# Optimization experiments

Hardware: AMD Instinct MI355X
Metric: run time of the kernel (lower is better)

Reference implementation:

```python
import jax, jax.numpy as jnp
import numpy as np

B, S, H = 2, 2048, 1024
N_HEADS = 16
HEAD_DIM = H // N_HEADS


def setup_inputs() -> dict:
    key = jax.random.key(0)
    ks = jax.random.split(key, 7)
    scale = 0.02
    return {
        "q": jax.random.normal(ks[0], (B, S, H), dtype=jnp.float32),
        "k": jax.random.normal(ks[1], (B, S, H), dtype=jnp.float32),
        "v": jax.random.normal(ks[2], (B, S, H), dtype=jnp.float32),
        "Wq": jax.random.normal(ks[3], (H, H), dtype=jnp.float32) * scale,
        "Wk": jax.random.normal(ks[4], (H, H), dtype=jnp.float32) * scale,
        "Wv": jax.random.normal(ks[5], (H, H), dtype=jnp.float32) * scale,
        "Wo": jax.random.normal(ks[6], (H, H), dtype=jnp.float32) * scale,
    }


def reference(q, k, v, Wq, Wk, Wv, Wo):
    b, i, _ = q.shape
    _, j, _ = k.shape
    # torch.nn.Linear(bias=False): y = x @ W.T
    qp = q @ Wq.T
    kp = k @ Wk.T
    vp = v @ Wv.T
    # NOTE: original uses .view(b, n_heads, i, head_dim) with NO transpose,
    # i.e. a raw reshape of the (b, i, hidden) layout. Replicate exactly.
    qh = qp.reshape(b, N_HEADS, i, HEAD_DIM)
    kh = kp.reshape(b, N_HEADS, j, HEAD_DIM)
    vh = vp.reshape(b, N_HEADS, j, HEAD_DIM)
    attn_score = jnp.einsum("bnid,bnjd->bnij", qh, kh) / (HEAD_DIM ** 0.5)
    attn_weight = jax.nn.softmax(attn_score, axis=3)
    x = jnp.einsum("bnij,bnjd->bnid", attn_weight, vh)  # [b, n, i, d]
    # rearrange 'b n i d -> b i (n d)'
    x = jnp.transpose(x, (0, 2, 1, 3)).reshape(b, i, H)
    out = x @ Wo.T
    return (out, attn_weight)
```

## Files before the change

kernel.cpp:

```cpp
#include <hip/hip_runtime.h>
#include <hip/hip_bf16.h>

#define DEVI __device__ __forceinline__

constexpr int kS  = 2048;
constexpr int kH  = 1024;
constexpr int kD  = 64;
constexpr int kBS = 4096;
constexpr int kHeadEls = kS * kD;

typedef __attribute__((ext_vector_type(4))) float f32x4;
typedef __attribute__((ext_vector_type(8))) __bf16 bf16x8;
typedef __attribute__((ext_vector_type(8))) unsigned short u16x8;
typedef __attribute__((ext_vector_type(2))) unsigned int u32x2;

DEVI unsigned short f2bf(float f) {
  unsigned int u = __builtin_bit_cast(unsigned int, f);
  u = u + 0x7FFFu + ((u >> 16) & 1u);
  return (unsigned short)(u >> 16);
}
DEVI float fast_exp2(float x) { float r; asm("v_exp_f32 %0, %1" : "=v"(r) : "v"(x)); return r; }
DEVI unsigned int cvt_pk(float lo, float hi) {
  unsigned int r; asm("v_cvt_pk_bf16_f32 %0, %1, %2" : "=v"(r) : "v"(lo), "v"(hi)); return r;
}
DEVI bf16x8 cvt8(const f32x4 a, const f32x4 b) {
  union { unsigned int u[4]; bf16x8 v; } r;
  r.u[0] = cvt_pk(a[0], a[1]); r.u[1] = cvt_pk(a[2], a[3]);
  r.u[2] = cvt_pk(b[0], b[1]); r.u[3] = cvt_pk(b[2], b[3]);
  return r.v;
}
DEVI float bf2f(unsigned int lo16) {
  return __builtin_bit_cast(float, lo16 << 16);
}

#define GLDS16(g, l) __builtin_amdgcn_global_load_lds( \
    (const __attribute__((address_space(1))) void*)(g), \
    (__attribute__((address_space(3))) void*)(l), 16, 0, 0)

__global__ __launch_bounds__(256) void cvt_all(
    const float* __restrict__ q, const float* __restrict__ k, const float* __restrict__ v,
    const float* __restrict__ Wq, const float* __restrict__ Wk, const float* __restrict__ Wv,
    unsigned short* __restrict__ stash)
{
  const int z = blockIdx.y, x = blockIdx.x;
  const float* s;
  unsigned short* d;
  size_t i;
  if (x < 2048) {
    s = z == 0 ? q : z == 1 ? k : v;
    d = stash + (size_t)z * 4194304;
    i = ((size_t)x * 256 + threadIdx.x) * 8;
  } else {
    s = z == 0 ? Wq : z == 1 ? Wk : Wv;
    d = stash + (size_t)12582912 + (size_t)z * 1048576;
    i = ((size_t)(x - 2048) * 256 + threadIdx.x) * 8;
  }
  f32x4 a = *(const f32x4*)(s + i);
  f32x4 b = *(const f32x4*)(s + i + 4);
  union { unsigned int u[4]; u16x8 v; } r;
  r.u[0] = cvt_pk(a[0], a[1]); r.u[1] = cvt_pk(a[2], a[3]);
  r.u[2] = cvt_pk(b[0], b[1]); r.u[3] = cvt_pk(b[2], b[3]);
  *(u16x8*)(d + i) = r.v;
}

__global__ __launch_bounds__(256, 3) void gemm_p(
    const unsigned short* __restrict__ Aq, const unsigned short* __restrict__ Ak,
    const unsigned short* __restrict__ Av,
    const unsigned short* __restrict__ Bq, const unsigned short* __restrict__ Bk,
    const unsigned short* __restrict__ Bv,
    unsigned short* __restrict__ Cq, unsigned short* __restrict__ Ck,
    unsigned short* __restrict__ Cv)
{
  constexpr int K = kH;
  __shared__ __align__(16) unsigned char As[2][8192];
  __shared__ __align__(16) unsigned char Bs[2][8192];

  const int z = blockIdx.z;
  const unsigned short* Ap = z == 0 ? Aq : z == 1 ? Ak : Av;
  const unsigned short* Bp = z == 0 ? Bq : z == 1 ? Bk : Bv;
  unsigned short*       Cp = z == 0 ? Cq : z == 1 ? Ck : Cv;

  const int tid  = threadIdx.x;
  const int lane = tid & 63, wv = tid >> 6;
  const int l15  = lane & 15, lg = lane >> 4;
  const int m0 = blockIdx.y * 128, n0 = blockIdx.x * 128;
  const int wM = (wv & 1) * 64, wN = (wv >> 1) * 64;

  const char* aSrc[2];
  const char* bSrc[2];
#pragma unroll
  for (int c = 0; c < 2; ++c) {
    const int row = c * 64 + (tid >> 2);
    const int cb  = ((tid & 3) * 16) ^ (((row >> 1) & 3) << 4);
    aSrc[c] = (const char*)Ap + ((size_t)(m0 + row) * K) * 2 + cb;
    bSrc[c] = (const char*)Bp + ((size_t)(n0 + row) * K) * 2 + cb;
  }

  int aoff[4], boff[4];
#pragma unroll
  for (int t = 0; t < 4; ++t) {
    const int rA = wM + t * 16 + l15;
    aoff[t] = rA * 64 + ((lg * 16) ^ (((rA >> 1) & 3) << 4));
    const int rB = wN + t * 16 + l15;
    boff[t] = rB * 64 + ((lg * 16) ^ (((rB >> 1) & 3) << 4));
  }

  f32x4 acc[4][4];
#pragma unroll
  for (int i = 0; i < 4; ++i)
#pragma unroll
    for (int j = 0; j < 4; ++j) acc[i][j] = {0.f, 0.f, 0.f, 0.f};

  auto STG = [&](int kk, int bb) {
#pragma unroll
    for (int c = 0; c < 2; ++c) {
      GLDS16(aSrc[c] + (size_t)kk * 2, &As[bb][c * 4096 + wv * 1024]);
      GLDS16(bSrc[c] + (size_t)kk * 2, &Bs[bb][c * 4096 + wv * 1024]);
    }
  };

  STG(0, 0);
  __syncthreads();
  int cur = 0;
  for (int t = 0; t < K / 32; ++t) {
    if (t < K / 32 - 1) STG((t + 1) * 32, cur ^ 1);
    bf16x8 af[4], bfr[4];
#pragma unroll
    for (int x = 0; x < 4; ++x) {
      af[x]  = *(const bf16x8*)&As[cur][aoff[x]];
      bfr[x] = *(const bf16x8*)&Bs[cur][boff[x]];
    }
#pragma unroll
    for (int mt = 0; mt < 4; ++mt)
#pragma unroll
      for (int nt = 0; nt < 4; ++nt)
        acc[mt][nt] = __builtin_amdgcn_mfma_f32_16x16x32_bf16(af[mt], bfr[nt], acc[mt][nt], 0, 0, 0);
    __syncthreads();
    cur ^= 1;
  }

  const bool vmode = (z == 2);
#pragma unroll
  for (int mt = 0; mt < 4; ++mt)
#pragma unroll
    for (int nt = 0; nt < 4; ++nt)
#pragma unroll
      for (int r = 0; r < 4; ++r) {
        const int row = m0 + wM + mt * 16 + lg * 4 + r;
        const int col = n0 + wN + nt * 16 + l15;
        const unsigned short hv = f2bf(acc[mt][nt][r]);
        if (!vmode) {
          Cp[(size_t)row * kH + col] = hv;
        } else {
          const int bn = row >> 7;
          const int j  = ((row & 127) << 4) | (col >> 6);
          const int d  = col & 63;
          Cp[(size_t)bn * kHeadEls + (size_t)d * kS + j] = hv;
        }
      }
}

__global__ __launch_bounds__(256, 3) void gemm_f(
    const unsigned short* __restrict__ Ap, const float* __restrict__ Bp,
    float* __restrict__ Cp)
{
  constexpr int K = kH;
  __shared__ __align__(16) unsigned char As[2][8192];
  __shared__ __align__(16) unsigned char Bs[2][8192];

  const int tid  = threadIdx.x;
  const int lane = tid & 63, wv = tid >> 6;
  const int l15  = lane & 15, lg = lane >> 4;
  const int m0 = blockIdx.y * 128, n0 = blockIdx.x * 64;
  const int wM = (wv & 1) * 64, wN = (wv >> 1) * 32;

  const char* aSrc[2];
#pragma unroll
  for (int c = 0; c < 2; ++c) {
    const int row = c * 64 + (tid >> 2);
    const int cb  = ((tid & 3) * 16) ^ (((row >> 1) & 3) << 4);
    aSrc[c] = (const char*)Ap + ((size_t)(m0 + row) * K) * 2 + cb;
  }
  const char* bSrc[2];
#pragma unroll
  for (int c = 0; c < 2; ++c) {
    const int row = c * 32 + (tid >> 3);
    const int cb  = ((tid & 7) * 16) ^ ((row & 7) << 4);
    bSrc[c] = (const char*)Bp + ((size_t)(n0 + row) * K) * 4 + cb;
  }

  int aoff[4], boff[2];
#pragma unroll
  for (int t = 0; t < 4; ++t) {
    const int rA = wM + t * 16 + l15;
    aoff[t] = rA * 64 + ((lg * 16) ^ (((rA >> 1) & 3) << 4));
  }
#pragma unroll
  for (int t = 0; t < 2; ++t) {
    const int rB = wN + t * 16 + l15;
    boff[t] = rB * 128 + ((lg * 32) ^ ((rB & 7) << 4));
  }

  f32x4 acc[4][2];
#pragma unroll
  for (int i = 0; i < 4; ++i)
#pragma unroll
    for (int j = 0; j < 2; ++j) acc[i][j] = {0.f, 0.f, 0.f, 0.f};

  auto STG = [&](int kk, int bb) {
#pragma unroll
    for (int c = 0; c < 2; ++c) {
      GLDS16(aSrc[c] + (size_t)kk * 2, &As[bb][c * 4096 + wv * 1024]);
      GLDS16(bSrc[c] + (size_t)kk * 4, &Bs[bb][c * 4096 + wv * 1024]);
    }
  };

  STG(0, 0);
  __syncthreads();
  int cur = 0;
  for (int t = 0; t < K / 32; ++t) {
    if (t < K / 32 - 1) STG((t + 1) * 32, cur ^ 1);
    bf16x8 af[4], bfr[2];
#pragma unroll
    for (int x = 0; x < 4; ++x)
      af[x] = *(const bf16x8*)&As[cur][aoff[x]];
#pragma unroll
    for (int x = 0; x < 2; ++x) {
      f32x4 q0 = *(const f32x4*)&Bs[cur][boff[x]];
      f32x4 q1 = *(const f32x4*)&Bs[cur][boff[x] ^ 16];
      bfr[x] = cvt8(q0, q1);
    }
#pragma unroll
    for (int mt = 0; mt < 4; ++mt)
#pragma unroll
      for (int nt = 0; nt < 2; ++nt)
        acc[mt][nt] = __builtin_amdgcn_mfma_f32_16x16x32_bf16(af[mt], bfr[nt], acc[mt][nt], 0, 0, 0);
    __syncthreads();
    cur ^= 1;
  }

#pragma unroll
  for (int mt = 0; mt < 4; ++mt)
#pragma unroll
    for (int nt = 0; nt < 2; ++nt)
#pragma unroll
      for (int r = 0; r < 4; ++r) {
        const int row = m0 + wM + mt * 16 + lg * 4 + r;
        const int col = n0 + wN + nt * 16 + l15;
        __builtin_nontemporal_store(acc[mt][nt][r], Cp + (size_t)row * kH + col);
      }
}

__global__ __launch_bounds__(256, 2) void attn_rs(
    const unsigned short* __restrict__ QP,
    const unsigned short* __restrict__ KP,
    float* __restrict__ rsout)
{
  __shared__ __align__(16) unsigned short Kb[2][4096];

  const int tid  = threadIdx.x;
  const int lane = tid & 63, wv = tid >> 6;
  const int l15  = lane & 15, lg = lane >> 4;
  const int f = blockIdx.x;
  const int x = f & 7, r = f >> 3;
  const int bn = (r >> 4) * 8 + x;
  const int i0 = (r & 15) * 128;

  const char* Khb = (const char*)(KP + (size_t)bn * kHeadEls);
  const unsigned short* Qh = QP + (size_t)bn * kHeadEls;

  int kbase[2];
#pragma unroll
  for (int p = 0; p < 2; ++p) {
    const int row = p * 32 + (tid >> 3);
    kbase[p] = row * 128 + (((tid & 7) * 16) ^ ((row & 7) << 4));
  }
  auto STAGE = [&](int j0, int bb) {
#pragma unroll
    for (int p = 0; p < 2; ++p)
      GLDS16(Khb + (size_t)j0 * 128 + kbase[p], (char*)Kb[bb] + p * 4096 + tid * 16);
  };

  int koff[4][2];
#pragma unroll
  for (int ct = 0; ct < 4; ++ct) {
    const int rK = ct * 16 + l15;
#pragma unroll
    for (int h = 0; h < 2; ++h)
      koff[ct][h] = rK * 128 + ((h * 64 + lg * 16) ^ ((rK & 7) << 4));
  }

  bf16x8 qf[2][2];
#pragma unroll
  for (int m = 0; m < 2; ++m) {
    const int qr = i0 + wv * 32 + m * 16 + l15;
#pragma unroll
    for (int h = 0; h < 2; ++h)
      qf[m][h] = *(const bf16x8*)(Qh + (size_t)qr * kD + h * 32 + lg * 8);
  }
  const float cexp = 0.18033688011112042f;

  float rs[2] = {0.f, 0.f};
  STAGE(0, 0);
  __syncthreads();
  int cur = 0;
  for (int t = 0; t < 32; ++t) {
    if (t < 31) STAGE((t + 1) * 64, cur ^ 1);
#pragma unroll
    for (int ct = 0; ct < 4; ++ct) {
      const bf16x8 kb0 = *(const bf16x8*)((const char*)Kb[cur] + koff[ct][0]);
      const bf16x8 kb1 = *(const bf16x8*)((const char*)Kb[cur] + koff[ct][1]);
#pragma unroll
      for (int m = 0; m < 2; ++m) {
        f32x4 s = {0.f, 0.f, 0.f, 0.f};
        s = __builtin_amdgcn_mfma_f32_16x16x32_bf16(kb0, qf[m][0], s, 0, 0, 0);
        s = __builtin_amdgcn_mfma_f32_16x16x32_bf16(kb1, qf[m][1], s, 0, 0, 0);
        const float w0 = fast_exp2(s[0] * cexp), w1 = fast_exp2(s[1] * cexp);
        const float w2 = fast_exp2(s[2] * cexp), w3 = fast_exp2(s[3] * cexp);
        rs[m] += (w0 + w1) + (w2 + w3);
      }
    }
    __syncthreads();
    cur ^= 1;
  }
#pragma unroll
  for (int m = 0; m < 2; ++m) {
    rs[m] += __shfl_xor(rs[m], 16, 64);
    rs[m] += __shfl_xor(rs[m], 32, 64);
  }
  if (lg == 0) {
#pragma unroll
    for (int m = 0; m < 2; ++m)
      rsout[(size_t)bn * kS + i0 + wv * 32 + m * 16 + l15] = rs[m];
  }
}

__global__ __launch_bounds__(256, 3) void attn_main(
    const unsigned short* __restrict__ QP,
    const unsigned short* __restrict__ KP,
    const unsigned short* __restrict__ VPT,
    const float* __restrict__ rsb,
    float* __restrict__ AW,
    unsigned short* __restrict__ XB)
{
  __shared__ __align__(16) unsigned short Kb[2][4096];
  __shared__ __align__(16) unsigned short Vb[2][4096];
  __shared__ __align__(16) unsigned short Ws[8192];

  const int tid  = threadIdx.x;
  const int lane = tid & 63, wv = tid >> 6;
  const int l15  = lane & 15, lg = lane >> 4;
  const int f = blockIdx.x;
  const int x = f & 7, r = f >> 3;
  const int bn = (r >> 4) * 8 + x;
  const int i0 = (r & 15) * 128;
  const int b = bn >> 4, n = bn & 15;

  const char* Khb = (const char*)(KP + (size_t)bn * kHeadEls);
  const char* Vhb = (const char*)(VPT + (size_t)bn * kHeadEls);
  const unsigned short* Qh = QP + (size_t)bn * kHeadEls;

  int kbase[2], vbase[2];
#pragma unroll
  for (int p = 0; p < 2; ++p) {
    const int row = p * 32 + (tid >> 3);
    const int sw  = ((tid & 7) * 16) ^ ((row & 7) << 4);
    kbase[p] = row * 128 + sw;
    vbase[p] = row * 4096 + sw;
  }
  auto STAGE_KV = [&](int j0, int bb) {
#pragma unroll
    for (int p = 0; p < 2; ++p) {
      GLDS16(Khb + (size_t)j0 * 128 + kbase[p], (char*)Kb[bb] + p * 4096 + tid * 16);
      GLDS16(Vhb + (size_t)j0 * 2 + vbase[p],   (char*)Vb[bb] + p * 4096 + tid * 16);
    }
  };

  int koff[4][2], voff[2][4], wswr[2][4], wsrd[2][2];
#pragma unroll
  for (int ct = 0; ct < 4; ++ct) {
    const int rK = ct * 16 + l15;
#pragma unroll
    for (int h = 0; h < 2; ++h)
      koff[ct][h] = rK * 128 + ((h * 64 + lg * 16) ^ ((rK & 7) << 4));
  }
#pragma unroll
  for (int jc = 0; jc < 2; ++jc)
#pragma unroll
    for (int dt = 0; dt < 4; ++dt) {
      const int d = dt * 16 + l15;
      voff[jc][dt] = d * 128 + ((jc * 64 + lg * 16) ^ ((d & 7) << 4));
    }
#pragma unroll
  for (int m = 0; m < 2; ++m) {
    const int rw = wv * 32 + m * 16 + l15;
#pragma unroll
    for (int ct = 0; ct < 4; ++ct)
      wswr[m][ct] = rw * 128 + ((ct * 32 + lg * 8) ^ ((rw & 7) << 4));
#pragma unroll
    for (int jc = 0; jc < 2; ++jc)
      wsrd[m][jc] = rw * 128 + ((jc * 64 + lg * 16) ^ ((rw & 7) << 4));
  }

  int awrd[8];
  float* awp[8];
#pragma unroll
  for (int u = 0; u < 8; ++u) {
    const int rw = wv * 32 + u * 4 + lg;
    awrd[u] = rw * 128 + ((l15 * 8) ^ ((rw & 7) << 4));
    awp[u]  = AW + ((size_t)bn * kS + i0 + rw) * kS + l15 * 4;
  }

  bf16x8 qf[2][2];
  float inv[2];
#pragma unroll
  for (int m = 0; m < 2; ++m) {
    const int qr = i0 + wv * 32 + m * 16 + l15;
#pragma unroll
    for (int h = 0; h < 2; ++h)
      qf[m][h] = *(const bf16x8*)(Qh + (size_t)qr * kD + h * 32 + lg * 8);
    inv[m] = 1.0f / rsb[(size_t)bn * kS + qr];
  }
  const float cexp = 0.18033688011112042f;

  f32x4 pv[2][4];
#pragma unroll
  for (int m = 0; m < 2; ++m)
#pragma unroll
    for (int dt = 0; dt < 4; ++dt) pv[m][dt] = {0.f, 0.f, 0.f, 0.f};

  STAGE_KV(0, 0);
  asm volatile("s_waitcnt vmcnt(0) lgkmcnt(0)" ::: "memory");
  __builtin_amdgcn_sched_barrier(0);
  __builtin_amdgcn_s_barrier();

  int cur = 0;
  for (int t = 0; t < 32; ++t) {
    if (t < 31) STAGE_KV((t + 1) * 64, cur ^ 1);
    __builtin_amdgcn_sched_barrier(0);
#pragma unroll
    for (int ct = 0; ct < 4; ++ct) {
      const bf16x8 kb0 = *(const bf16x8*)((const char*)Kb[cur] + koff[ct][0]);
      const bf16x8 kb1 = *(const bf16x8*)((const char*)Kb[cur] + koff[ct][1]);
#pragma unroll
      for (int m = 0; m < 2; ++m) {
        f32x4 s = {0.f, 0.f, 0.f, 0.f};
        s = __builtin_amdgcn_mfma_f32_16x16x32_bf16(kb0, qf[m][0], s, 0, 0, 0);
        s = __builtin_amdgcn_mfma_f32_16x16x32_bf16(kb1, qf[m][1], s, 0, 0, 0);
        f32x4 w;
#pragma unroll
        for (int r2 = 0; r2 < 4; ++r2) w[r2] = fast_exp2(s[r2] * cexp) * inv[m];
        u32x2 pk; pk[0] = cvt_pk(w[0], w[1]); pk[1] = cvt_pk(w[2], w[3]);
        *(u32x2*)((char*)Ws + wswr[m][ct]) = pk;
      }
    }
#pragma unroll
    for (int jc = 0; jc < 2; ++jc) {
      const bf16x8 pa0 = *(const bf16x8*)((const char*)Ws + wsrd[0][jc]);
      const bf16x8 pa1 = *(const bf16x8*)((const char*)Ws + wsrd[1][jc]);
#pragma unroll
      for (int dt = 0; dt < 4; ++dt) {
        const bf16x8 vf = *(const bf16x8*)((const char*)Vb[cur] + voff[jc][dt]);
        pv[0][dt] = __builtin_amdgcn_mfma_f32_16x16x32_bf16(pa0, vf, pv[0][dt], 0, 0, 0);
        pv[1][dt] = __builtin_amdgcn_mfma_f32_16x16x32_bf16(pa1, vf, pv[1][dt], 0, 0, 0);
      }
    }
#pragma unroll
    for (int u = 0; u < 8; ++u) {
      const u32x2 pk = *(const u32x2*)((const char*)Ws + awrd[u]);
      f32x4 w;
      w[0] = bf2f(pk[0] & 0xFFFFu);
      w[1] = bf2f(pk[0] >> 16);
      w[2] = bf2f(pk[1] & 0xFFFFu);
      w[3] = bf2f(pk[1] >> 16);
      __builtin_nontemporal_store(w, (f32x4*)(awp[u] + t * 64));
    }
    if (t < 31) {
      asm volatile("s_waitcnt vmcnt(8) lgkmcnt(0)" ::: "memory");
      __builtin_amdgcn_sched_barrier(0);
      __builtin_amdgcn_s_barrier();
    }
    cur ^= 1;
  }

#pragma unroll
  for (int m = 0; m < 2; ++m)
#pragma unroll
    for (int dt = 0; dt < 4; ++dt)
#pragma unroll
      for (int r2 = 0; r2 < 4; ++r2) {
        const int row = b * kS + i0 + wv * 32 + m * 16 + lg * 4 + r2;
        const int col = n * 64 + dt * 16 + l15;
        XB[(size_t)row * kH + col] = f2bf(pv[m][dt][r2]);
      }
}

extern "C" void kernel_launch(void* const* d_in, const int* in_sizes, int n_in,
                              void* d_out, int out_size, void* d_ws, size_t ws_size,
                              hipStream_t stream) {
  const float* q  = (const float*)d_in[0];
  const float* k  = (const float*)d_in[1];
  const float* v  = (const float*)d_in[2];
  const float* Wq = (const float*)d_in[3];
  const float* Wk = (const float*)d_in[4];
  const float* Wv = (const float*)d_in[5];
  const float* Wo = (const float*)d_in[6];

  float* out = (float*)d_out;
  float* aw  = out + (size_t)kBS * kH;
  float* rsb = out;

  unsigned short* QP  = (unsigned short*)d_ws;
  unsigned short* KP  = QP  + (size_t)kBS * kH;
  unsigned short* VPT = KP  + (size_t)kBS * kH;
  unsigned short* XB  = VPT + (size_t)kBS * kH;

  unsigned short* stash = (unsigned short*)aw;
  unsigned short* QB  = stash;
  unsigned short* KB  = stash + (size_t)4194304;
  unsigned short* VB  = stash + (size_t)8388608;
  unsigned short* Wqb = stash + (size_t)12582912;
  unsigned short* Wkb = stash + (size_t)13631488;
  unsigned short* Wvb = stash + (size_t)14680064;

  cvt_all<<<dim3(2560, 3), 256, 0, stream>>>(q, k, v, Wq, Wk, Wv, stash);
  gemm_p<<<dim3(8, 32, 3), 256, 0, stream>>>(QB, KB, VB, Wqb, Wkb, Wvb, QP, KP, VPT);
  attn_rs<<<dim3(512), 256, 0, stream>>>(QP, KP, rsb);
  attn_main<<<dim3(512), 256, 0, stream>>>(QP, KP, VPT, rsb, aw, XB);
  gemm_f<<<dim3(16, 32), 256, 0, stream>>>(XB, Wo, out);
}
```

Measured before the change: 247.5 us.

## Fuse row-sum pass into attention kernel and triple-buffer GEMM staging

Merges the separate softmax row-sum kernel into the main attention kernel. Each block now first sweeps K in 128-row tiles through a triple-buffered LDS region to compute its own row sums, then reuses the same shared memory for the K/V/weights pass, which removes one launch and the global round trip of the row sums. Both projection GEMMs switch from double to triple buffering, issuing loads two tiles ahead and waiting with a partial vmcnt instead of a full __syncthreads. The cost is higher LDS use (48KB per block), which may reduce occupancy, and a longer serial section per attention block.

```diff
diff --git a/kernel.cpp b/kernel.cpp
--- a/kernel.cpp
+++ b/kernel.cpp
@@ -36,6 +36,11 @@
 #define GLDS16(g, l) __builtin_amdgcn_global_load_lds( \
     (const __attribute__((address_space(1))) void*)(g), \
     (__attribute__((address_space(3))) void*)(l), 16, 0, 0)
+
+#define WAIT_VM(n) do { \
+    asm volatile("s_waitcnt vmcnt(" #n ") lgkmcnt(0)" ::: "memory"); \
+    __builtin_amdgcn_sched_barrier(0); \
+    __builtin_amdgcn_s_barrier(); } while (0)
 
 __global__ __launch_bounds__(256) void cvt_all(
     const float* __restrict__ q, const float* __restrict__ k, const float* __restrict__ v,
@@ -72,8 +77,8 @@
     unsigned short* __restrict__ Cv)
 {
   constexpr int K = kH;
-  __shared__ __align__(16) unsigned char As[2][8192];
-  __shared__ __align__(16) unsigned char Bs[2][8192];
+  __shared__ __align__(16) unsigned char As[3][8192];
+  __shared__ __align__(16) unsigned char Bs[3][8192];
 
   const int z = blockIdx.z;
   const unsigned short* Ap = z == 0 ? Aq : z == 1 ? Ak : Av;
@@ -119,11 +124,11 @@
     }
   };
 
-  STG(0, 0);
-  __syncthreads();
-  int cur = 0;
-  for (int t = 0; t < K / 32; ++t) {
-    if (t < K / 32 - 1) STG((t + 1) * 32, cur ^ 1);
+  STG(0, 0); STG(32, 1);
+  WAIT_VM(4);
+  int cur = 0, nx2 = 2;
+  for (int t = 0; t < 32; ++t) {
+    if (t < 30) STG((t + 2) * 32, nx2);
     bf16x8 af[4], bfr[4];
 #pragma unroll
     for (int x = 0; x < 4; ++x) {
@@ -135,8 +140,12 @@
 #pragma unroll
       for (int nt = 0; nt < 4; ++nt)
         acc[mt][nt] = __builtin_amdgcn_mfma_f32_16x16x32_bf16(af[mt], bfr[nt], acc[mt][nt], 0, 0, 0);
-    __syncthreads();
-    cur ^= 1;
+    if (t < 31) {
+      if (t < 30) WAIT_VM(4);
+      else        WAIT_VM(0);
+    }
+    cur = cur == 2 ? 0 : cur + 1;
+    nx2 = nx2 == 2 ? 0 : nx2 + 1;
   }
 
   const bool vmode = (z == 2);
@@ -165,8 +174,8 @@
     float* __restrict__ Cp)
 {
   constexpr int K = kH;
-  __shared__ __align__(16) unsigned char As[2][8192];
-  __shared__ __align__(16) unsigned char Bs[2][8192];
+  __shared__ __align__(16) unsigned char As[3][8192];
+  __shared__ __align__(16) unsigned char Bs[3][8192];
 
   const int tid  = threadIdx.x;
   const int lane = tid & 63, wv = tid >> 6;
@@ -215,11 +224,11 @@
     }
   };
 
-  STG(0, 0);
-  __syncthreads();
-  int cur = 0;
-  for (int t = 0; t < K / 32; ++t) {
-    if (t < K / 32 - 1) STG((t + 1) * 32, cur ^ 1);
+  STG(0, 0); STG(32, 1);
+  WAIT_VM(4);
+  int cur = 0, nx2 = 2;
+  for (int t = 0; t < 32; ++t) {
+    if (t < 30) STG((t + 2) * 32, nx2);
     bf16x8 af[4], bfr[2];
 #pragma unroll
     for (int x = 0; x < 4; ++x)
@@ -235,8 +244,12 @@
 #pragma unroll
       for (int nt = 0; nt < 2; ++nt)
         acc[mt][nt] = __builtin_amdgcn_mfma_f32_16x16x32_bf16(af[mt], bfr[nt], acc[mt][nt], 0, 0, 0);
-    __syncthreads();
-    cur ^= 1;
+    if (t < 31) {
+      if (t < 30) WAIT_VM(4);
+      else        WAIT_VM(0);
+    }
+    cur = cur == 2 ? 0 : cur + 1;
+    nx2 = nx2 == 2 ? 0 : nx2 + 1;
   }
 
 #pragma unroll
@@ -251,101 +264,14 @@
       }
 }
 
-__global__ __launch_bounds__(256, 2) void attn_rs(
-    const unsigned short* __restrict__ QP,
-    const unsigned short* __restrict__ KP,
-    float* __restrict__ rsout)
-{
-  __shared__ __align__(16) unsigned short Kb[2][4096];
-
-  const int tid  = threadIdx.x;
-  const int lane = tid & 63, wv = tid >> 6;
-  const int l15  = lane & 15, lg = lane >> 4;
-  const int f = blockIdx.x;
-  const int x = f & 7, r = f >> 3;
-  const int bn = (r >> 4) * 8 + x;
-  const int i0 = (r & 15) * 128;
-
-  const char* Khb = (const char*)(KP + (size_t)bn * kHeadEls);
-  const unsigned short* Qh = QP + (size_t)bn * kHeadEls;
-
-  int kbase[2];
-#pragma unroll
-  for (int p = 0; p < 2; ++p) {
-    const int row = p * 32 + (tid >> 3);
-    kbase[p] = row * 128 + (((tid & 7) * 16) ^ ((row & 7) << 4));
-  }
-  auto STAGE = [&](int j0, int bb) {
-#pragma unroll
-    for (int p = 0; p < 2; ++p)
-      GLDS16(Khb + (size_t)j0 * 128 + kbase[p], (char*)Kb[bb] + p * 4096 + tid * 16);
-  };
-
-  int koff[4][2];
-#pragma unroll
-  for (int ct = 0; ct < 4; ++ct) {
-    const int rK = ct * 16 + l15;
-#pragma unroll
-    for (int h = 0; h < 2; ++h)
-      koff[ct][h] = rK * 128 + ((h * 64 + lg * 16) ^ ((rK & 7) << 4));
-  }
-
-  bf16x8 qf[2][2];
-#pragma unroll
-  for (int m = 0; m < 2; ++m) {
-    const int qr = i0 + wv * 32 + m * 16 + l15;
-#pragma unroll
-    for (int h = 0; h < 2; ++h)
-      qf[m][h] = *(const bf16x8*)(Qh + (size_t)qr * kD + h * 32 + lg * 8);
-  }
-  const float cexp = 0.18033688011112042f;
-
-  float rs[2] = {0.f, 0.f};
-  STAGE(0, 0);
-  __syncthreads();
-  int cur = 0;
-  for (int t = 0; t < 32; ++t) {
-    if (t < 31) STAGE((t + 1) * 64, cur ^ 1);
-#pragma unroll
-    for (int ct = 0; ct < 4; ++ct) {
-      const bf16x8 kb0 = *(const bf16x8*)((const char*)Kb[cur] + koff[ct][0]);
-      const bf16x8 kb1 = *(const bf16x8*)((const char*)Kb[cur] + koff[ct][1]);
-#pragma unroll
-      for (int m = 0; m < 2; ++m) {
-        f32x4 s = {0.f, 0.f, 0.f, 0.f};
-        s = __builtin_amdgcn_mfma_f32_16x16x32_bf16(kb0, qf[m][0], s, 0, 0, 0);
-        s = __builtin_amdgcn_mfma_f32_16x16x32_bf16(kb1, qf[m][1], s, 0, 0, 0);
-        const float w0 = fast_exp2(s[0] * cexp), w1 = fast_exp2(s[1] * cexp);
-        const float w2 = fast_exp2(s[2] * cexp), w3 = fast_exp2(s[3] * cexp);
-        rs[m] += (w0 + w1) + (w2 + w3);
-      }
-    }
-    __syncthreads();
-    cur ^= 1;
-  }
-#pragma unroll
-  for (int m = 0; m < 2; ++m) {
-    rs[m] += __shfl_xor(rs[m], 16, 64);
-    rs[m] += __shfl_xor(rs[m], 32, 64);
-  }
-  if (lg == 0) {
-#pragma unroll
-    for (int m = 0; m < 2; ++m)
-      rsout[(size_t)bn * kS + i0 + wv * 32 + m * 16 + l15] = rs[m];
-  }
-}
-
-__global__ __launch_bounds__(256, 3) void attn_main(
+__global__ __launch_bounds__(256, 3) void attn_fused(
     const unsigned short* __restrict__ QP,
     const unsigned short* __restrict__ KP,
     const unsigned short* __restrict__ VPT,
-    const float* __restrict__ rsb,
     float* __restrict__ AW,
     unsigned short* __restrict__ XB)
 {
-  __shared__ __align__(16) unsigned short Kb[2][4096];
-  __shared__ __align__(16) unsigned short Vb[2][4096];
-  __shared__ __align__(16) unsigned short Ws[8192];
+  __shared__ __align__(16) unsigned char SM[49152];
 
   const int tid  = threadIdx.x;
   const int lane = tid & 63, wv = tid >> 6;
@@ -360,6 +286,73 @@
   const char* Vhb = (const char*)(VPT + (size_t)bn * kHeadEls);
   const unsigned short* Qh = QP + (size_t)bn * kHeadEls;
 
+  bf16x8 qf[2][2];
+#pragma unroll
+  for (int m = 0; m < 2; ++m) {
+    const int qr = i0 + wv * 32 + m * 16 + l15;
+#pragma unroll
+    for (int h = 0; h < 2; ++h)
+      qf[m][h] = *(const bf16x8*)(Qh + (size_t)qr * kD + h * 32 + lg * 8);
+  }
+  const float cexp = 0.18033688011112042f;
+
+  int kb1[4];
+#pragma unroll
+  for (int p = 0; p < 4; ++p) {
+    const int row = p * 32 + (tid >> 3);
+    kb1[p] = row * 128 + (((tid & 7) * 16) ^ ((row & 7) << 4));
+  }
+  auto STAGE1 = [&](int j0, int bb) {
+#pragma unroll
+    for (int p = 0; p < 4; ++p)
+      GLDS16(Khb + (size_t)j0 * 128 + kb1[p], SM + bb * 16384 + p * 4096 + tid * 16);
+  };
+
+  float rs[2] = {0.f, 0.f};
+  STAGE1(0, 0); STAGE1(128, 1);
+  WAIT_VM(4);
+  int c1 = 0, n1 = 2;
+  for (int t = 0; t < 16; ++t) {
+    if (t < 14) STAGE1((t + 2) * 128, n1);
+    const char* kb = (const char*)SM + c1 * 16384;
+#pragma unroll
+    for (int ct = 0; ct < 8; ++ct) {
+      const int rK = ct * 16 + l15;
+      const int sw = (rK & 7) << 4;
+      const bf16x8 k0 = *(const bf16x8*)(kb + rK * 128 + ((lg * 16) ^ sw));
+      const bf16x8 k1 = *(const bf16x8*)(kb + rK * 128 + ((64 + lg * 16) ^ sw));
+#pragma unroll
+      for (int m = 0; m < 2; ++m) {
+        f32x4 s = {0.f, 0.f, 0.f, 0.f};
+        s = __builtin_amdgcn_mfma_f32_16x16x32_bf16(k0, qf[m][0], s, 0, 0, 0);
+        s = __builtin_amdgcn_mfma_f32_16x16x32_bf16(k1, qf[m][1], s, 0, 0, 0);
+        const float w0 = fast_exp2(s[0] * cexp), w1 = fast_exp2(s[1] * cexp);
+        const float w2 = fast_exp2(s[2] * cexp), w3 = fast_exp2(s[3] * cexp);
+        rs[m] += (w0 + w1) + (w2 + w3);
+      }
+    }
+    if (t < 15) {
+      if (t < 14) WAIT_VM(4);
+      else        WAIT_VM(0);
+    }
+    c1 = c1 == 2 ? 0 : c1 + 1;
+    n1 = n1 == 2 ? 0 : n1 + 1;
+  }
+#pragma unroll
+  for (int m = 0; m < 2; ++m) {
+    rs[m] += __shfl_xor(rs[m], 16, 64);
+    rs[m] += __shfl_xor(rs[m], 32, 64);
+  }
+  float inv[2];
+#pragma unroll
+  for (int m = 0; m < 2; ++m) inv[m] = 1.0f / rs[m];
+
+  __syncthreads();
+
+  char* const Kb2 = (char*)SM;
+  char* const Vb2 = (char*)SM + 16384;
+  char* const Wsb = (char*)SM + 32768;
+
   int kbase[2], vbase[2];
 #pragma unroll
   for (int p = 0; p < 2; ++p) {
@@ -371,8 +364,8 @@
   auto STAGE_KV = [&](int j0, int bb) {
 #pragma unroll
     for (int p = 0; p < 2; ++p) {
-      GLDS16(Khb + (size_t)j0 * 128 + kbase[p], (char*)Kb[bb] + p * 4096 + tid * 16);
-      GLDS16(Vhb + (size_t)j0 * 2 + vbase[p],   (char*)Vb[bb] + p * 4096 + tid * 16);
+      GLDS16(Khb + (size_t)j0 * 128 + kbase[p], Kb2 + bb * 8192 + p * 4096 + tid * 16);
+      GLDS16(Vhb + (size_t)j0 * 2 + vbase[p],   Vb2 + bb * 8192 + p * 4096 + tid * 16);
     }
   };
 
@@ -411,18 +404,6 @@
     awp[u]  = AW + ((size_t)bn * kS + i0 + rw) * kS + l15 * 4;
   }
 
-  bf16x8 qf[2][2];
-  float inv[2];
-#pragma unroll
-  for (int m = 0; m < 2; ++m) {
-    const int qr = i0 + wv * 32 + m * 16 + l15;
-#pragma unroll
-    for (int h = 0; h < 2; ++h)
-      qf[m][h] = *(const bf16x8*)(Qh + (size_t)qr * kD + h * 32 + lg * 8);
-    inv[m] = 1.0f / rsb[(size_t)bn * kS + qr];
-  }
-  const float cexp = 0.18033688011112042f;
-
   f32x4 pv[2][4];
 #pragma unroll
   for (int m = 0; m < 2; ++m)
@@ -430,9 +411,7 @@
     for (int dt = 0; dt < 4; ++dt) pv[m][dt] = {0.f, 0.f, 0.f, 0.f};
 
   STAGE_KV(0, 0);
-  asm volatile("s_waitcnt vmcnt(0) lgkmcnt(0)" ::: "memory");
-  __builtin_amdgcn_sched_barrier(0);
-  __builtin_amdgcn_s_barrier();
+  WAIT_VM(0);
 
   int cur = 0;
   for (int t = 0; t < 32; ++t) {
@@ -440,8 +419,8 @@
     __builtin_amdgcn_sched_barrier(0);
 #pragma unroll
     for (int ct = 0; ct < 4; ++ct) {
-      const bf16x8 kb0 = *(const bf16x8*)((const char*)Kb[cur] + koff[ct][0]);
-      const bf16x8 kb1 = *(const bf16x8*)((const char*)Kb[cur] + koff[ct][1]);
+      const bf16x8 kb0 = *(const bf16x8*)(Kb2 + cur * 8192 + koff[ct][0]);
+      const bf16x8 kb1 = *(const bf16x8*)(Kb2 + cur * 8192 + koff[ct][1]);
 #pragma unroll
       for (int m = 0; m < 2; ++m) {
         f32x4 s = {0.f, 0.f, 0.f, 0.f};
@@ -451,23 +430,23 @@
 #pragma unroll
         for (int r2 = 0; r2 < 4; ++r2) w[r2] = fast_exp2(s[r2] * cexp) * inv[m];
         u32x2 pk; pk[0] = cvt_pk(w[0], w[1]); pk[1] = cvt_pk(w[2], w[3]);
-        *(u32x2*)((char*)Ws + wswr[m][ct]) = pk;
+        *(u32x2*)(Wsb + wswr[m][ct]) = pk;
       }
     }
 #pragma unroll
     for (int jc = 0; jc < 2; ++jc) {
-      const bf16x8 pa0 = *(const bf16x8*)((const char*)Ws + wsrd[0][jc]);
-      const bf16x8 pa1 = *(const bf16x8*)((const char*)Ws + wsrd[1][jc]);
+      const bf16x8 pa0 = *(const bf16x8*)(Wsb + wsrd[0][jc]);
+      const bf16x8 pa1 = *(const bf16x8*)(Wsb + wsrd[1][jc]);
 #pragma unroll
       for (int dt = 0; dt < 4; ++dt) {
-        const bf16x8 vf = *(const bf16x8*)((const char*)Vb[cur] + voff[jc][dt]);
+        const bf16x8 vf = *(const bf16x8*)(Vb2 + cur * 8192 + voff[jc][dt]);
         pv[0][dt] = __builtin_amdgcn_mfma_f32_16x16x32_bf16(pa0, vf, pv[0][dt], 0, 0, 0);
         pv[1][dt] = __builtin_amdgcn_mfma_f32_16x16x32_bf16(pa1, vf, pv[1][dt], 0, 0, 0);
       }
     }
 #pragma unroll
     for (int u = 0; u < 8; ++u) {
-      const u32x2 pk = *(const u32x2*)((const char*)Ws + awrd[u]);
+      const u32x2 pk = *(const u32x2*)(Wsb + awrd[u]);
       f32x4 w;
       w[0] = bf2f(pk[0] & 0xFFFFu);
       w[1] = bf2f(pk[0] >> 16);
@@ -475,11 +454,7 @@
       w[3] = bf2f(pk[1] >> 16);
       __builtin_nontemporal_store(w, (f32x4*)(awp[u] + t * 64));
     }
-    if (t < 31) {
-      asm volatile("s_waitcnt vmcnt(8) lgkmcnt(0)" ::: "memory");
-      __builtin_amdgcn_sched_barrier(0);
-      __builtin_amdgcn_s_barrier();
-    }
+    if (t < 31) WAIT_VM(8);
     cur ^= 1;
   }
 
@@ -508,7 +483,6 @@
 
   float* out = (float*)d_out;
   float* aw  = out + (size_t)kBS * kH;
-  float* rsb = out;
 
   unsigned short* QP  = (unsigned short*)d_ws;
   unsigned short* KP  = QP  + (size_t)kBS * kH;
@@ -525,7 +499,6 @@
 
   cvt_all<<<dim3(2560, 3), 256, 0, stream>>>(q, k, v, Wq, Wk, Wv, stash);
   gemm_p<<<dim3(8, 32, 3), 256, 0, stream>>>(QB, KB, VB, Wqb, Wkb, Wvb, QP, KP, VPT);
-  attn_rs<<<dim3(512), 256, 0, stream>>>(QP, KP, rsb);
-  attn_main<<<dim3(512), 256, 0, stream>>>(QP, KP, VPT, rsb, aw, XB);
+  attn_fused<<<dim3(512), 256, 0, stream>>>(QP, KP, VPT, aw, XB);
   gemm_f<<<dim3(16, 32), 256, 0, stream>>>(XB, Wo, out);
 }
```

New measurement: 234.1 us. 1.06x faster.
